# Optimization experiments

Measured on AMD Instinct MI355X. Metric: run time of the kernel, lower is better.

Reference implementation:

```python
import jax, jax.numpy as jnp
import numpy as np

T, B, F, CONTEXT = 2048, 16, 1024, 20


def setup_inputs() -> dict:
    key = jax.random.key(0)
    k1, k2 = jax.random.split(key)
    x = jax.random.normal(k1, (T, B, F), dtype=jnp.float32)
    stdv = 1.0 / np.sqrt(CONTEXT + 1)
    weight = jax.random.uniform(k2, (F, CONTEXT + 1), dtype=jnp.float32,
                                minval=-stdv, maxval=stdv)
    return {"x": x, "weight": weight, "tail_padding": 1}


def reference(x, weight, tail_padding):
    # x: (T, B, F); weight: (F, context+1)
    context = weight.shape[1] - 1
    if tail_padding:
        pad = jnp.zeros((context,) + x.shape[1:], dtype=x.dtype)
        x = jnp.concatenate([x, pad], axis=0)
    seq_len = x.shape[0] - context  # == T when tail_padding
    # Causal-lookahead depthwise conv over time:
    # y[t, b, f] = sum_k x[t+k, b, f] * weight[f, k]
    y = jnp.zeros((seq_len,) + x.shape[1:], dtype=x.dtype)
    for k in range(context + 1):
        y = y + x[k:k + seq_len] * weight[:, k]
    return y
```

## Files before the change

### kernel.cpp

```cpp
#include <hip/hip_runtime.h>


constexpr int T = 2048;
constexpr int B = 16;
constexpr int F = 1024;
constexpr int K = 21;
constexpr int BF = B * F;
constexpr int CV = BF / 4;
constexpr int TCHUNK = 64;
constexpr int UNROLL = 4;
constexpr int BLOCK = 256;

static_assert(TCHUNK % UNROLL == 0, "");
static_assert(T % TCHUNK == 0, "");
static_assert(CV % BLOCK == 0, "");
static_assert(TCHUNK >= K - 1, "preload guard elision requires TCHUNK >= K-1");

__device__ __forceinline__ float4 fma4(float4 a, float4 w, float4 c) {
    return make_float4(fmaf(a.x, w.x, c.x), fmaf(a.y, w.y, c.y),
                       fmaf(a.z, w.z, c.z), fmaf(a.w, w.w, c.w));
}

__global__ __launch_bounds__(BLOCK)
__attribute__((amdgpu_waves_per_eu(2, 2)))
void lookahead_kernel(const float4* __restrict__ x,
                      const float* __restrict__ weight,
                      float4* __restrict__ y)
{
    const int cv = blockIdx.x * BLOCK + threadIdx.x;
    const int f0 = (cv * 4) & (F - 1);
    const int t0 = blockIdx.y * TCHUNK;

    float4 w[K];
    const float* wp = weight + f0 * K;
    #pragma unroll
    for (int k = 0; k < K; ++k)
        w[k] = make_float4(wp[k], wp[K + k], wp[2 * K + k], wp[3 * K + k]);

    #pragma unroll
    for (int k = 0; k < K; ++k)
        asm volatile("" : "+v"(w[k].x), "+v"(w[k].y), "+v"(w[k].z), "+v"(w[k].w));

    const float4* xc = x + cv;
    float4*       yc = y + cv;

    float4 win[K - 1 + UNROLL];
    float4 nxt[UNROLL];

    #pragma unroll
    for (int k = 0; k < K - 1; ++k)
        win[k] = xc[(t0 + k) * CV];

    #pragma unroll
    for (int u = 0; u < UNROLL; ++u) {
        const int tt = t0 + (K - 1) + u;
        nxt[u] = (tt < T) ? xc[tt * CV] : make_float4(0.f, 0.f, 0.f, 0.f);
    }

    for (int tb = 0; tb < TCHUNK; tb += UNROLL) {
        const int t = t0 + tb;

        #pragma unroll
        for (int u = 0; u < UNROLL; ++u)
            win[K - 1 + u] = nxt[u];

        if (tb + UNROLL < TCHUNK) {
            #pragma unroll
            for (int u = 0; u < UNROLL; ++u) {
                const int tt = t + UNROLL + (K - 1) + u;
                nxt[u] = (tt < T) ? xc[tt * CV]
                                  : make_float4(0.f, 0.f, 0.f, 0.f);
            }
        }

        #pragma unroll
        for (int u = 0; u < UNROLL; ++u) {
            float4 acc = make_float4(0.f, 0.f, 0.f, 0.f);
            #pragma unroll
            for (int k = 0; k < K; ++k)
                acc = fma4(win[u + k], w[k], acc);
            yc[(t + u) * CV] = acc;
        }

        #pragma unroll
        for (int k = 0; k < K - 1; ++k)
            win[k] = win[k + UNROLL];
    }
}

extern "C" void kernel_launch(void* const* d_in, const int* in_sizes, int n_in,
                              void* d_out, int out_size, void* d_ws, size_t ws_size,
                              hipStream_t stream) {
    const float4* x     = (const float4*)d_in[0];
    const float* weight = (const float*)d_in[1];
    float4* y = (float4*)d_out;

    dim3 grid(CV / BLOCK, T / TCHUNK);
    lookahead_kernel<<<grid, dim3(BLOCK), 0, stream>>>(x, weight, y);
}
```

Baseline: 251.3 us.

## Stage weights in LDS, transposed by tap, instead of holding them in registers

Each block now stages the weights for a 512-feature segment into shared memory, laid out k-major. In the inner loop each weight float4 is read from LDS once per tap and reused across the four unrolled timesteps. The per-thread register array of 21 float4 weights and the fixed waves-per-EU attribute are gone, which frees VGPRs and should allow more occupancy to hide memory latency on this bandwidth-bound conv. The cost is a per-block staging loop, a barrier, and LDS reads in the hot loop.

```diff
diff --git a/kernel.cpp b/kernel.cpp
--- a/kernel.cpp
+++ b/kernel.cpp
@@ -7,14 +7,16 @@
 constexpr int K = 21;
 constexpr int BF = B * F;
 constexpr int CV = BF / 4;
+constexpr int FSEG = 512;
 constexpr int TCHUNK = 64;
 constexpr int UNROLL = 4;
 constexpr int BLOCK = 256;
+constexpr int WFLOATS = FSEG * K;
 
 static_assert(TCHUNK % UNROLL == 0, "");
 static_assert(T % TCHUNK == 0, "");
-static_assert(CV % BLOCK == 0, "");
 static_assert(TCHUNK >= K - 1, "preload guard elision requires TCHUNK >= K-1");
+static_assert(WFLOATS % BLOCK == 0, "staging loop has no remainder");
 
 __device__ __forceinline__ float4 fma4(float4 a, float4 w, float4 c) {
     return make_float4(fmaf(a.x, w.x, c.x), fmaf(a.y, w.y, c.y),
@@ -22,30 +24,44 @@
 }
 
 __global__ __launch_bounds__(BLOCK)
-__attribute__((amdgpu_waves_per_eu(2, 2)))
 void lookahead_kernel(const float4* __restrict__ x,
                       const float* __restrict__ weight,
                       float4* __restrict__ y)
 {
-    const int cv = blockIdx.x * BLOCK + threadIdx.x;
-    const int f0 = (cv * 4) & (F - 1);
-    const int t0 = blockIdx.y * TCHUNK;
+    __shared__ float wlds[WFLOATS];
 
-    float4 w[K];
-    const float* wp = weight + f0 * K;
-    #pragma unroll
-    for (int k = 0; k < K; ++k)
-        w[k] = make_float4(wp[k], wp[K + k], wp[2 * K + k], wp[3 * K + k]);
+    const int bx    = blockIdx.x;
+    const int fseg  = bx & 1;
+    const int b0    = (bx >> 1) * 2;
+    const int fbase = fseg * FSEG;
+    const int tid   = threadIdx.x;
 
-    #pragma unroll
-    for (int k = 0; k < K; ++k)
-        asm volatile("" : "+v"(w[k].x), "+v"(w[k].y), "+v"(w[k].z), "+v"(w[k].w));
+    {
+        const float* wg = weight + fbase * K;
+        #pragma unroll
+        for (int j = 0; j < WFLOATS / BLOCK; ++j) {
+            const int idx = j * BLOCK + tid;
+            const float v = wg[idx];
+            const int fl  = idx / K;
+            const int k   = idx - fl * K;
+            wlds[k * FSEG + fl] = v;
+        }
+    }
+    __syncthreads();
 
-    const float4* xc = x + cv;
-    float4*       yc = y + cv;
+    const int b   = b0 + (tid >> 7);
+    const int fl  = (tid * 4) & (FSEG - 1);
+    const int cv  = (b * F + fbase + fl) >> 2;
+    const int flq = fl >> 2;
+    const int t0  = blockIdx.y * TCHUNK;
+
+    const float4* xc  = x + cv;
+    float4*       yc  = y + cv;
+    const float4* wl4 = (const float4*)wlds;
 
     float4 win[K - 1 + UNROLL];
     float4 nxt[UNROLL];
+    const float4 zero = make_float4(0.f, 0.f, 0.f, 0.f);
 
     #pragma unroll
     for (int k = 0; k < K - 1; ++k)
@@ -54,7 +70,7 @@
     #pragma unroll
     for (int u = 0; u < UNROLL; ++u) {
         const int tt = t0 + (K - 1) + u;
-        nxt[u] = (tt < T) ? xc[tt * CV] : make_float4(0.f, 0.f, 0.f, 0.f);
+        nxt[u] = (tt < T) ? xc[tt * CV] : zero;
     }
 
     for (int tb = 0; tb < TCHUNK; tb += UNROLL) {
@@ -68,19 +84,25 @@
             #pragma unroll
             for (int u = 0; u < UNROLL; ++u) {
                 const int tt = t + UNROLL + (K - 1) + u;
-                nxt[u] = (tt < T) ? xc[tt * CV]
-                                  : make_float4(0.f, 0.f, 0.f, 0.f);
+                nxt[u] = (tt < T) ? xc[tt * CV] : zero;
             }
         }
 
+        float4 acc[UNROLL];
         #pragma unroll
-        for (int u = 0; u < UNROLL; ++u) {
-            float4 acc = make_float4(0.f, 0.f, 0.f, 0.f);
+        for (int u = 0; u < UNROLL; ++u) acc[u] = zero;
+
+        #pragma unroll
+        for (int k = 0; k < K; ++k) {
+            const float4 wk = wl4[k * (FSEG / 4) + flq];
             #pragma unroll
-            for (int k = 0; k < K; ++k)
-                acc = fma4(win[u + k], w[k], acc);
-            yc[(t + u) * CV] = acc;
+            for (int u = 0; u < UNROLL; ++u)
+                acc[u] = fma4(win[u + k], wk, acc[u]);
         }
+
+        #pragma unroll
+        for (int u = 0; u < UNROLL; ++u)
+            yc[(t + u) * CV] = acc[u];
 
         #pragma unroll
         for (int k = 0; k < K - 1; ++k)
@@ -95,6 +117,6 @@
     const float* weight = (const float*)d_in[1];
     float4* y = (float4*)d_out;
 
-    dim3 grid(CV / BLOCK, T / TCHUNK);
+    dim3 grid(BF / (BLOCK * 4), T / TCHUNK);
     lookahead_kernel<<<grid, dim3(BLOCK), 0, stream>>>(x, weight, y);
 }
```

After: 244.5 us. 2.7% less time.
